# Optimization experiments

Measured on AMD Instinct MI355X. Metric: run time of the kernel, lower is better.

The kernel has to match this reference:

```python
import jax, jax.numpy as jnp
import numpy as np

ALPHA = 1.0

def setup_inputs() -> dict:
    key = jax.random.key(0)
    k1, k2, k3, k4 = jax.random.split(key, 4)
    B, N, D = 2048, 32768, 128
    return {
        "anchor": jax.random.normal(k1, (B, D), dtype=jnp.float32),
        "positive": jax.random.normal(k2, (B, D), dtype=jnp.float32),
        "negative": jax.random.normal(k3, (N, D), dtype=jnp.float32),
        "r_score": jax.random.normal(k4, (B, 1), dtype=jnp.float32),
    }

def reference(anchor, positive, negative, r_score):
    # pos_sim: [B,1] elementwise dot per row
    pos_sim = jnp.sum(anchor * positive, axis=1, keepdims=True)
    # neg_mul: [B,N] score matrix; row-wise stable logsumexp -> [B,1]
    neg_mul = jnp.matmul(anchor, negative.T)
    neg_sim = jax.scipy.special.logsumexp(neg_mul, axis=1, keepdims=True)
    loss = jax.nn.relu(neg_sim - pos_sim + r_score + ALPHA)
    return jnp.mean(loss)
```

## Files before the change

kernel.cpp:

```cpp
#include <hip/hip_runtime.h>
#include <hip/hip_bf16.h>


#define B_ROWS 2048
#define N_NEG  32768
#define DIM    128
#define LOG2E  1.4426950408889634f
#define LN2    0.6931471805599453f

typedef __bf16 bf16x8 __attribute__((ext_vector_type(8)));
typedef float  f32x4  __attribute__((ext_vector_type(4)));

static __device__ inline unsigned short f2bf(float f) {
    union { float f; unsigned u; } v; v.f = f;
    unsigned r = v.u + 0x7FFF + ((v.u >> 16) & 1);
    return (unsigned short)(r >> 16);
}

static __device__ inline void load_lds16(const void* g, void* s) {
    __builtin_amdgcn_global_load_lds(
        (const __attribute__((address_space(1))) void*)g,
        (__attribute__((address_space(3))) void*)s,
        16, 0, 0);
}

__global__ void prep(const float* __restrict__ anchor,
                     const float* __restrict__ positive,
                     const float* __restrict__ neg,
                     unsigned short* __restrict__ a_bf,
                     unsigned short* __restrict__ n_bf,
                     float* __restrict__ pos_sim,
                     float* __restrict__ sumexp) {
    int t = threadIdx.x;
    if (blockIdx.x < 256) {
        int row = blockIdx.x * 8 + (t >> 5);
        int c4  = (t & 31) * 4;
        const float4 a4 = *(const float4*)(anchor   + row * DIM + c4);
        const float4 p4 = *(const float4*)(positive + row * DIM + c4);
        float dot = a4.x * p4.x + a4.y * p4.y + a4.z * p4.z + a4.w * p4.w;
        ushort4 ab;
        ab.x = f2bf(a4.x * LOG2E); ab.y = f2bf(a4.y * LOG2E);
        ab.z = f2bf(a4.z * LOG2E); ab.w = f2bf(a4.w * LOG2E);
        *(ushort4*)(a_bf + row * DIM + c4) = ab;
        #pragma unroll
        for (int m = 1; m <= 16; m <<= 1) dot += __shfl_xor(dot, m, 64);
        if ((t & 31) == 0) { pos_sim[row] = dot; sumexp[row] = 0.0f; }
    } else {
        int i = (blockIdx.x - 256) * 256 + t;
        #pragma unroll
        for (int k = 0; k < 4; k++) {
            int idx = i + k * (1024 * 256);
            float4 v = *(const float4*)(neg + (size_t)idx * 4);
            ushort4 o;
            o.x = f2bf(v.x); o.y = f2bf(v.y); o.z = f2bf(v.z); o.w = f2bf(v.w);
            *(ushort4*)(n_bf + (size_t)idx * 4) = o;
        }
    }
}

#define CHUNK 1024
#define TSTEPS (CHUNK / 128)

__global__ __launch_bounds__(256, 2) void fused_gemm_lse(
        const unsigned short* __restrict__ A,
        const unsigned short* __restrict__ Nb,
        float* __restrict__ sumexp) {
    __shared__ unsigned short lds[2][128 * 128];

    const int bid     = blockIdx.x;
    const int rowTile = bid & 15;
    const int chunk   = bid >> 4;
    const int wave = threadIdx.x >> 6, lane = threadIdx.x & 63;
    const int wr = wave >> 1, wc = wave & 1;
    const int q = lane >> 4, c = lane & 15;
    const int lrow = lane >> 4;
    const int lchk = lane & 15;

    const unsigned short* Ag = A + rowTile * (128 * DIM);
    const unsigned short* Bg = Nb + (size_t)(chunk * CHUNK) * DIM;

    #pragma unroll
    for (int i = 0; i < 8; i++) {
        int off = wave * 4096 + i * 512;
        int r   = (off >> 7) + lrow;
        int gofs = r * DIM + ((lchk ^ (r & 7)) << 3);
        load_lds16(Ag + gofs, &lds[0][off]);
        load_lds16(Bg + gofs, &lds[1][off]);
    }
    asm volatile("s_waitcnt vmcnt(0)" ::: "memory");
    __syncthreads();

    int swz[4];
    #pragma unroll
    for (int k = 0; k < 4; k++) swz[k] = (((k * 4 + q) ^ (c & 7)) << 3);

    bf16x8 af[4][4];
    #pragma unroll
    for (int i = 0; i < 4; i++) {
        int row = wr * 64 + i * 16 + c;
        #pragma unroll
        for (int k = 0; k < 4; k++)
            af[i][k] = *(const bf16x8*)&lds[0][row * DIM + swz[k]];
    }
    __syncthreads();

    const f32x4 zero4 = {0.f, 0.f, 0.f, 0.f};
    f32x4 sumacc[4] = {zero4, zero4, zero4, zero4};

    for (int t = 0; t < TSTEPS; t++) {
        const int cur = 1 - (t & 1);
        const int nxt = t & 1;
        if (t + 1 < TSTEPS) {
            const unsigned short* Bn = Bg + (size_t)(t + 1) * 128 * DIM;
            #pragma unroll
            for (int i = 0; i < 8; i++) {
                int off = wave * 4096 + i * 512;
                int r   = (off >> 7) + lrow;
                int gofs = r * DIM + ((lchk ^ (r & 7)) << 3);
                load_lds16(Bn + gofs, &lds[nxt][off]);
            }
        }
        #pragma unroll
        for (int j = 0; j < 4; j++) {
            int brow = wc * 64 + j * 16 + c;
            bf16x8 bf[4];
            #pragma unroll
            for (int k = 0; k < 4; k++)
                bf[k] = *(const bf16x8*)&lds[cur][brow * DIM + swz[k]];
            #pragma unroll
            for (int i = 0; i < 4; i++) {
                f32x4 acc = __builtin_amdgcn_mfma_f32_16x16x32_bf16(af[i][0], bf[0], zero4, 0, 0, 0);
                acc = __builtin_amdgcn_mfma_f32_16x16x32_bf16(af[i][1], bf[1], acc, 0, 0, 0);
                acc = __builtin_amdgcn_mfma_f32_16x16x32_bf16(af[i][2], bf[2], acc, 0, 0, 0);
                acc = __builtin_amdgcn_mfma_f32_16x16x32_bf16(af[i][3], bf[3], acc, 0, 0, 0);
                sumacc[i][0] += __builtin_amdgcn_exp2f(acc[0]);
                sumacc[i][1] += __builtin_amdgcn_exp2f(acc[1]);
                sumacc[i][2] += __builtin_amdgcn_exp2f(acc[2]);
                sumacc[i][3] += __builtin_amdgcn_exp2f(acc[3]);
            }
        }
        if (t + 1 < TSTEPS) {
            asm volatile("s_waitcnt vmcnt(0)" ::: "memory");
            __syncthreads();
        }
    }

    #pragma unroll
    for (int i = 0; i < 4; i++) {
        #pragma unroll
        for (int r = 0; r < 4; r++) {
            float v = sumacc[i][r];
            v += __shfl_xor(v, 1, 64);
            v += __shfl_xor(v, 2, 64);
            v += __shfl_xor(v, 4, 64);
            v += __shfl_xor(v, 8, 64);
            if ((lane & 15) == 0) {
                int row = rowTile * 128 + wr * 64 + i * 16 + q * 4 + r;
                atomicAdd(&sumexp[row], v);
            }
        }
    }
}

__global__ void finalize(const float* __restrict__ sumexp,
                         const float* __restrict__ pos_sim,
                         const float* __restrict__ r_score,
                         float* __restrict__ out) {
    __shared__ float red[4];
    int t = threadIdx.x;
    float acc = 0.0f;
    #pragma unroll
    for (int i = 0; i < 8; i++) {
        int row = t + i * 256;
        float lse  = __log2f(sumexp[row]) * LN2;
        float loss = lse - pos_sim[row] + r_score[row] + 1.0f;
        acc += fmaxf(loss, 0.0f);
    }
    #pragma unroll
    for (int m = 1; m <= 32; m <<= 1) acc += __shfl_xor(acc, m, 64);
    if ((t & 63) == 0) red[t >> 6] = acc;
    __syncthreads();
    if (t == 0) out[0] = (red[0] + red[1] + red[2] + red[3]) * (1.0f / (float)B_ROWS);
}

extern "C" void kernel_launch(void* const* d_in, const int* in_sizes, int n_in,
                              void* d_out, int out_size, void* d_ws, size_t ws_size,
                              hipStream_t stream) {
    const float* anchor   = (const float*)d_in[0];
    const float* positive = (const float*)d_in[1];
    const float* negative = (const float*)d_in[2];
    const float* r_score  = (const float*)d_in[3];
    float* out = (float*)d_out;

    char* ws = (char*)d_ws;
    float* sumexp           = (float*)ws;
    float* pos_sim          = (float*)(ws + 8192);
    unsigned short* a_bf    = (unsigned short*)(ws + 16384);
    unsigned short* n_bf    = (unsigned short*)(ws + 16384 + 524288);

    prep<<<1280, 256, 0, stream>>>(anchor, positive, negative, a_bf, n_bf, pos_sim, sumexp);
    fused_gemm_lse<<<512, 256, 0, stream>>>(a_bf, n_bf, sumexp);
    finalize<<<1, 256, 0, stream>>>(sumexp, pos_sim, r_score, out);
}
```

Measured before the change: 95.46 us.

## Deepen B-tile prefetch pipeline with split LDS slots and partial vmcnt waits

```diff
diff --git a/kernel.cpp b/kernel.cpp
--- a/kernel.cpp
+++ b/kernel.cpp
@@ -65,7 +65,7 @@
         const unsigned short* __restrict__ A,
         const unsigned short* __restrict__ Nb,
         float* __restrict__ sumexp) {
-    __shared__ unsigned short lds[2][128 * 128];
+    __shared__ unsigned short lds[4 * 8192];
 
     const int bid     = blockIdx.x;
     const int rowTile = bid & 15;
@@ -79,16 +79,23 @@
     const unsigned short* Ag = A + rowTile * (128 * DIM);
     const unsigned short* Bg = Nb + (size_t)(chunk * CHUNK) * DIM;
 
-    #pragma unroll
-    for (int i = 0; i < 8; i++) {
-        int off = wave * 4096 + i * 512;
-        int r   = (off >> 7) + lrow;
-        int gofs = r * DIM + ((lchk ^ (r & 7)) << 3);
-        load_lds16(Ag + gofs, &lds[0][off]);
-        load_lds16(Bg + gofs, &lds[1][off]);
-    }
-    asm volatile("s_waitcnt vmcnt(0)" ::: "memory");
-    __syncthreads();
+#define STAGE_TILE(gbase, tt)                                                  \
+    {                                                                          \
+        const int h_ = wave >> 1;                                              \
+        const int s_ = (2 * (tt) + 2 + h_) & 3;                                \
+        _Pragma("unroll")                                                      \
+        for (int i_ = 0; i_ < 8; i_++) {                                       \
+            int rloc_ = (wave & 1) * 32 + i_ * 4;        \
+            int rg_   = h_ * 64 + rloc_ + lrow;         \
+            int gofs_ = rg_ * DIM + ((lchk ^ (rg_ & 7)) << 3);                 \
+            load_lds16((gbase) + gofs_, &lds[s_ * 8192 + rloc_ * DIM]);        \
+        }                                                                      \
+    }
+
+    STAGE_TILE(Ag, -1);
+    STAGE_TILE(Bg, 0);
+    asm volatile("s_waitcnt vmcnt(8)" ::: "memory");
+    __builtin_amdgcn_s_barrier();
 
     int swz[4];
     #pragma unroll
@@ -97,36 +104,32 @@
     bf16x8 af[4][4];
     #pragma unroll
     for (int i = 0; i < 4; i++) {
-        int row = wr * 64 + i * 16 + c;
+        int row = i * 16 + c;
         #pragma unroll
         for (int k = 0; k < 4; k++)
-            af[i][k] = *(const bf16x8*)&lds[0][row * DIM + swz[k]];
-    }
-    __syncthreads();
+            af[i][k] = *(const bf16x8*)&lds[wr * 8192 + row * DIM + swz[k]];
+    }
+    asm volatile("s_waitcnt lgkmcnt(0)" ::: "memory");
+    __builtin_amdgcn_s_barrier();
+
+    STAGE_TILE(Bg + 128 * DIM, 1);
 
     const f32x4 zero4 = {0.f, 0.f, 0.f, 0.f};
     f32x4 sumacc[4] = {zero4, zero4, zero4, zero4};
 
     for (int t = 0; t < TSTEPS; t++) {
-        const int cur = 1 - (t & 1);
-        const int nxt = t & 1;
-        if (t + 1 < TSTEPS) {
-            const unsigned short* Bn = Bg + (size_t)(t + 1) * 128 * DIM;
-            #pragma unroll
-            for (int i = 0; i < 8; i++) {
-                int off = wave * 4096 + i * 512;
-                int r   = (off >> 7) + lrow;
-                int gofs = r * DIM + ((lchk ^ (r & 7)) << 3);
-                load_lds16(Bn + gofs, &lds[nxt][off]);
-            }
-        }
+        if (t < TSTEPS - 1) asm volatile("s_waitcnt vmcnt(8)" ::: "memory");
+        else                asm volatile("s_waitcnt vmcnt(0)" ::: "memory");
+        __builtin_amdgcn_s_barrier();
+
+        const int sb = (2 * t + 2 + wc) & 3;
         #pragma unroll
         for (int j = 0; j < 4; j++) {
-            int brow = wc * 64 + j * 16 + c;
+            int brow = j * 16 + c;
             bf16x8 bf[4];
             #pragma unroll
             for (int k = 0; k < 4; k++)
-                bf[k] = *(const bf16x8*)&lds[cur][brow * DIM + swz[k]];
+                bf[k] = *(const bf16x8*)&lds[sb * 8192 + brow * DIM + swz[k]];
             #pragma unroll
             for (int i = 0; i < 4; i++) {
                 f32x4 acc = __builtin_amdgcn_mfma_f32_16x16x32_bf16(af[i][0], bf[0], zero4, 0, 0, 0);
@@ -139,11 +142,12 @@
                 sumacc[i][3] += __builtin_amdgcn_exp2f(acc[3]);
             }
         }
-        if (t + 1 < TSTEPS) {
-            asm volatile("s_waitcnt vmcnt(0)" ::: "memory");
-            __syncthreads();
-        }
-    }
+        asm volatile("s_waitcnt lgkmcnt(0)" ::: "memory");
+        __builtin_amdgcn_s_barrier();
+        if (t + 2 < TSTEPS)
+            STAGE_TILE(Bg + (size_t)(t + 2) * 128 * DIM, t + 2);
+    }
+#undef STAGE_TILE
 
     #pragma unroll
     for (int i = 0; i < 4; i++) {
```

After: 95.29 us. No clear change (-0.2%).
